# Kernel tuning notes

Hardware: AMD Instinct MI355X
Metric: run time of the kernel (lower is better)

Reference implementation:

```python
import jax, jax.numpy as jnp
import numpy as np

HID = 1024
DEPTH = 2

def _rhn_layer(x, Win, bin_, Wh, bh, Wt, bt):
    # x: [B, T, in]; returns outputs [B, T, H]
    B = x.shape[0]
    h0 = jnp.zeros((B, HID), dtype=x.dtype)
    xt = jnp.swapaxes(x, 0, 1)  # [T, B, in]

    def step(h_prev, x_t):
        h = x_t @ Win + bin_
        for i in range(DEPTH):
            t_gate = jax.nn.sigmoid(h @ Wt[i] + bt[i])
            h_layer = jnp.tanh(h @ Wh[i] + bh[i])
            h = t_gate * h_layer + (1.0 - t_gate) * h
        h_new = h + h_prev
        return h_new, h_new

    _, outs = jax.lax.scan(step, h0, xt)  # [T, B, H]
    return jnp.swapaxes(outs, 0, 1)


def setup_inputs() -> dict:
    key = jax.random.key(0)
    ks = jax.random.split(key, 16)
    B, T, IN, H, OUT = 64, 256, 128, HID, 128
    s = lambda fan_in: 1.0 / np.sqrt(fan_in)
    d = {}
    d["x"] = jax.random.normal(ks[0], (B, T, IN), dtype=jnp.float32)
    # layer 0 (input_size=IN)
    d["l0_Win"] = jax.random.uniform(ks[1], (IN, H), minval=-s(IN), maxval=s(IN))
    d["l0_bin"] = jax.random.uniform(ks[2], (H,), minval=-s(IN), maxval=s(IN))
    d["l0_Wh"] = jax.random.uniform(ks[3], (DEPTH, H, H), minval=-s(H), maxval=s(H))
    d["l0_bh"] = jax.random.uniform(ks[4], (DEPTH, H), minval=-s(H), maxval=s(H))
    d["l0_Wt"] = jax.random.uniform(ks[5], (DEPTH, H, H), minval=-s(H), maxval=s(H))
    d["l0_bt"] = jax.random.uniform(ks[6], (DEPTH, H), minval=-s(H), maxval=s(H))
    # layer 1 (input_size=H)
    d["l1_Win"] = jax.random.uniform(ks[7], (H, H), minval=-s(H), maxval=s(H))
    d["l1_bin"] = jax.random.uniform(ks[8], (H,), minval=-s(H), maxval=s(H))
    d["l1_Wh"] = jax.random.uniform(ks[9], (DEPTH, H, H), minval=-s(H), maxval=s(H))
    d["l1_bh"] = jax.random.uniform(ks[10], (DEPTH, H), minval=-s(H), maxval=s(H))
    d["l1_Wt"] = jax.random.uniform(ks[11], (DEPTH, H, H), minval=-s(H), maxval=s(H))
    d["l1_bt"] = jax.random.uniform(ks[12], (DEPTH, H), minval=-s(H), maxval=s(H))
    # final fc
    d["fc_W"] = jax.random.uniform(ks[13], (H, OUT), minval=-s(H), maxval=s(H))
    d["fc_b"] = jax.random.uniform(ks[14], (OUT,), minval=-s(H), maxval=s(H))
    return d


def reference(x, l0_Win, l0_bin, l0_Wh, l0_bh, l0_Wt, l0_bt,
              l1_Win, l1_bin, l1_Wh, l1_bh, l1_Wt, l1_bt, fc_W, fc_b):
    out = _rhn_layer(x, l0_Win, l0_bin, l0_Wh, l0_bh, l0_Wt, l0_bt)
    out = _rhn_layer(out, l1_Win, l1_bin, l1_Wh, l1_bh, l1_Wt, l1_bt)
    # forecast_horizon = 1 -> last time step only
    out = out[:, -1:, :] @ fc_W + fc_b  # [B, 1, OUT]
    return out
```

## Files before the change

kernel.cpp:

```cpp
#include <hip/hip_runtime.h>

typedef unsigned short u16;
typedef unsigned int u32;
typedef __bf16 bf16x8 __attribute__((ext_vector_type(8)));
typedef float floatx4 __attribute__((ext_vector_type(4)));

#define HID 1024
#define BATCH 64
#define SEQ 256
#define INDIM 128
#define OUTDIM 128
#define MROWS (BATCH*SEQ)

__device__ __forceinline__ float b2f(u16 u) {
    union { u32 u; float f; } v; v.u = ((u32)u) << 16; return v.f;
}
__device__ __forceinline__ u16 f2b(float f) {
    union { float f; u32 u; } v; v.f = f;
    u32 x = v.u;
    x += 0x7fffu + ((x >> 16) & 1u);
    return (u16)(x >> 16);
}
__device__ __forceinline__ float sigm(float x) { return 1.f / (1.f + __expf(-x)); }
__device__ __forceinline__ float tanh_f(float x) { return 2.f / (1.f + __expf(-2.f * x)) - 1.f; }

__device__ __forceinline__ void gld16(const u16* g, u16* l) {
    __builtin_amdgcn_global_load_lds(
        (const __attribute__((address_space(1))) void*)g,
        (__attribute__((address_space(3))) void*)l, 16, 0, 0);
}

__device__ __forceinline__ void bar_sync() {
    asm volatile("" ::: "memory");
    __builtin_amdgcn_s_barrier();
    asm volatile("" ::: "memory");
}
template <int N>
__device__ __forceinline__ void vm_bar() {
    asm volatile("s_waitcnt vmcnt(%0)" :: "n"(N) : "memory");
    __builtin_amdgcn_s_barrier();
    asm volatile("" ::: "memory");
}

__global__ void detect_dtype(const u16* __restrict__ w, int* __restrict__ flag) {
    __shared__ int s;
    if (threadIdx.x == 0) s = 0;
    __syncthreads();
    int bad = 0;
    for (int i = threadIdx.x; i < 4096; i += 256) {
        int e = (w[i] >> 7) & 0xff;
        if (e >= 127) bad = 1;
    }
    if (bad) atomicOr(&s, 1);
    __syncthreads();
    if (threadIdx.x == 0) *flag = s;
}

__device__ __forceinline__ int is_fp32(const u16* probe) {
    const int lane = threadIdx.x & 63;
    const int e = (probe[lane * 7] >> 7) & 0xff;
    return __ballot(e >= 127) != 0ULL;
}

struct CvtList { const void* s[7]; u16* d[7]; int n[7]; };

__global__ void convert7(CvtList C, const int* __restrict__ flag) {
    const int fp32 = *flag;
    const int z = blockIdx.y;
    const int n = C.n[z];
    const int stride = gridDim.x * 256;
    for (int i = blockIdx.x * 256 + threadIdx.x; i < n; i += stride) {
        u16 o;
        if (fp32) o = f2b(((const float*)C.s[z])[i]);
        else      o = ((const u16*)C.s[z])[i];
        C.d[z][i] = o;
    }
}

struct TListO {
    const void* s[10];
    u16*        d[10];
    int         R[10];
    int         Cc[10];
    long        off[10];
};

__global__ void transpose10(TListO L, const int* __restrict__ flag) {
    const int fp32 = *flag;
    const int z = blockIdx.z;
    const void* src = L.s[z];
    u16*        dst = L.d[z];
    const int R  = L.R[z];
    const int Cc = L.Cc[z];
    const long zo = L.off[z];
    const int tr = blockIdx.y * 32, tc = blockIdx.x * 32;
    if (tr >= R || tc >= Cc) return;
    __align__(16) __shared__ u16 t[32][33];
    const int tx = threadIdx.x, ty = threadIdx.y;
#pragma unroll
    for (int i = 0; i < 4; ++i) {
        const int r = ty + i * 8;
        const long e = zo + (long)(tr + r) * Cc + tc + tx;
        u16 v;
        if (fp32) v = f2b(((const float*)src)[e]);
        else      v = ((const u16*)src)[e];
        t[r][tx] = v;
    }
    __syncthreads();
#pragma unroll
    for (int i = 0; i < 4; ++i) {
        const int r = ty + i * 8;
        dst[(size_t)(tc + r) * R + tr + tx] = t[tx][r];
    }
}

__device__ __forceinline__ void tile_swizzle(int& m0, int& n0) {
    const int lin = blockIdx.y * gridDim.x + blockIdx.x;
    const int xcd = lin & 7;
    const int loc = lin >> 3;
    m0 = (xcd * 16 + (loc & 15)) * 128;
    n0 = (loc >> 4) * 128;
}

__device__ __forceinline__ void tile_swizzle8(int& m0, int& n0) {
    const int lin = blockIdx.x;
    const int xcd = lin & 7;
    const int loc = lin >> 3;
    m0 = (xcd * 8 + (loc & 7)) * 256;
    n0 = (loc >> 3) * 128;
}

__global__ __launch_bounds__(256, 2) void gemm128(
    const u16* __restrict__ A, const u16* __restrict__ BT,
    const u16* __restrict__ bias, u16* __restrict__ C,
    int M, int N, int K)
{
    __align__(16) __shared__ u16 As[128 * 64];
    __align__(16) __shared__ u16 Bs[128 * 64];

    const int tid  = threadIdx.x;
    const int lane = tid & 63;
    const int wid  = tid >> 6;
    const int wr   = wid >> 1;
    const int wc   = wid & 1;

    int m0, n0;
    tile_swizzle(m0, n0);

    floatx4 acc[4][4] = {};

    const int srow = lane >> 3;
    const int scol = 8 * ((lane & 7) ^ (lane >> 3));
    const int cb   = wid * 4;
    const u16* Ag[4]; const u16* Bg[4];
    u16 *Al[4], *Bl[4];
#pragma unroll
    for (int j = 0; j < 4; ++j) {
        const int c = cb + j;
        const int r = c * 8 + srow;
        Ag[j] = A  + (size_t)(m0 + r) * K + scol;
        Bg[j] = BT + (size_t)(n0 + r) * K + scol;
        Al[j] = As + c * 512;
        Bl[j] = Bs + c * 512;
    }

    const int quad = lane >> 4;
    const int l16  = lane & 15;
    const int swz  = l16 & 7;

    const int nk = K >> 6;
    for (int kt = 0; kt < nk; ++kt) {
        __syncthreads();
#pragma unroll
        for (int j = 0; j < 4; ++j) {
            gld16(Ag[j], Al[j]);  gld16(Bg[j], Bl[j]);
            Ag[j] += 64; Bg[j] += 64;
        }
        __syncthreads();

#pragma unroll
        for (int kk = 0; kk < 2; ++kk) {
            const int slot = ((kk * 4 + quad) ^ swz) * 8;
            bf16x8 af[4], bfr[4];
#pragma unroll
            for (int i = 0; i < 4; ++i) {
                af[i]  = *(const bf16x8*)(As + (wr * 64 + i * 16 + l16) * 64 + slot);
                bfr[i] = *(const bf16x8*)(Bs + (wc * 64 + i * 16 + l16) * 64 + slot);
            }
#pragma unroll
            for (int i = 0; i < 4; ++i)
#pragma unroll
                for (int j = 0; j < 4; ++j)
                    acc[i][j] = __builtin_amdgcn_mfma_f32_16x16x32_bf16(af[i], bfr[j], acc[i][j], 0, 0, 0);
        }
    }

#pragma unroll
    for (int i = 0; i < 4; ++i) {
        const int rowb = m0 + wr * 64 + i * 16 + quad * 4;
#pragma unroll
        for (int j = 0; j < 4; ++j) {
            const int col = n0 + wc * 64 + j * 16 + l16;
            const float bv = b2f(bias[col]);
#pragma unroll
            for (int r = 0; r < 4; ++r)
                C[(size_t)(rowb + r) * N + col] = f2b(acc[i][j][r] + bv);
        }
    }
}

__device__ __forceinline__ void hw8_mainloop(
    const u16* __restrict__ A, const u16* __restrict__ WtT, const u16* __restrict__ WhT,
    int m0, int n0, int K,
    floatx4 (&acct)[4][4], floatx4 (&acch)[4][4])
{
    __align__(16) __shared__ u16 lds[65536];

    const int tid  = threadIdx.x;
    const int lane = tid & 63;
    const int wid  = tid >> 6;
    const int wr   = wid >> 1;
    const int wc   = wid & 1;

    const int srow = lane >> 3;
    const int scol = 8 * ((lane & 7) ^ srow);

    const u16* Ag = A   + (size_t)(m0 + wid * 32 + srow) * K + scol;
    const u16* Tg = WtT + (size_t)(n0 + wid * 16 + srow) * K + scol;
    const u16* Hg = WhT + (size_t)(n0 + wid * 16 + srow) * K + scol;
    const size_t K8 = (size_t)K * 8;

    u16* dA = lds + wid * 2048;
    u16* dT = lds + 16384 + wid * 1024;
    u16* dH = lds + 24576 + wid * 1024;

    const int quad = lane >> 4;
    const int l16  = lane & 15;
    const int swz  = l16 & 7;
    const int s0 = (quad ^ swz) * 8;
    const int s1 = ((4 + quad) ^ swz) * 8;
    const int ra = wr * 64 + l16;
    const int rb = wc * 64 + l16;

    gld16(Tg,           dT);
    gld16(Tg +     K8,  dT + 512);
    gld16(Ag,           dA);
    gld16(Ag +     K8,  dA + 512);
    gld16(Ag + 2 * K8,  dA + 1024);
    gld16(Ag + 3 * K8,  dA + 1536);
    gld16(Hg,           dH);
    gld16(Hg +     K8,  dH + 512);
    Ag += 64; Tg += 64; Hg += 64;
    vm_bar<2>();

    const int nk = K >> 6;
    for (int kt = 0; kt < nk; ++kt) {
        const int  cur = kt & 1;
        const int  nb  = (cur ^ 1) * 32768;
        const bool pf  = (kt + 1 < nk);
        const u16* Sa = lds + cur * 32768;
        const u16* St = Sa + 16384;
        const u16* Sh = Sa + 24576;

        bf16x8 af0[4], af1[4], bq[4];

#pragma unroll
        for (int i = 0; i < 4; ++i) {
            af0[i] = *(const bf16x8*)(Sa + (ra + i * 16) * 64 + s0);
            bq[i]  = *(const bf16x8*)(St + (rb + i * 16) * 64 + s0);
        }
        if (pf) {
            gld16(Tg,      dT + nb);  gld16(Tg + K8, dT + nb + 512);
            gld16(Ag,      dA + nb);  gld16(Ag + K8, dA + nb + 512);
        }
        bar_sync();
        __builtin_amdgcn_s_setprio(1);
#pragma unroll
        for (int i = 0; i < 4; ++i)
#pragma unroll
            for (int j = 0; j < 4; ++j)
                acct[i][j] = __builtin_amdgcn_mfma_f32_16x16x32_bf16(af0[i], bq[j], acct[i][j], 0, 0, 0);
        __builtin_amdgcn_s_setprio(0);

#pragma unroll
        for (int i = 0; i < 4; ++i) {
            af1[i] = *(const bf16x8*)(Sa + (ra + i * 16) * 64 + s1);
            bq[i]  = *(const bf16x8*)(St + (rb + i * 16) * 64 + s1);
        }
        if (pf) {
            gld16(Ag + 2 * K8, dA + nb + 1024);
            gld16(Ag + 3 * K8, dA + nb + 1536);
            vm_bar<6>();
        } else {
            vm_bar<0>();
        }
        __builtin_amdgcn_s_setprio(1);
#pragma unroll
        for (int i = 0; i < 4; ++i)
#pragma unroll
            for (int j = 0; j < 4; ++j)
                acct[i][j] = __builtin_amdgcn_mfma_f32_16x16x32_bf16(af1[i], bq[j], acct[i][j], 0, 0, 0);
        __builtin_amdgcn_s_setprio(0);

#pragma unroll
        for (int i = 0; i < 4; ++i)
            bq[i] = *(const bf16x8*)(Sh + (rb + i * 16) * 64 + s0);
        bar_sync();
        __builtin_amdgcn_s_setprio(1);
#pragma unroll
        for (int i = 0; i < 4; ++i)
#pragma unroll
            for (int j = 0; j < 4; ++j)
                acch[i][j] = __builtin_amdgcn_mfma_f32_16x16x32_bf16(af0[i], bq[j], acch[i][j], 0, 0, 0);
        __builtin_amdgcn_s_setprio(0);

#pragma unroll
        for (int i = 0; i < 4; ++i)
            bq[i] = *(const bf16x8*)(Sh + (rb + i * 16) * 64 + s1);
        if (pf) {
            gld16(Hg,      dH + nb);
            gld16(Hg + K8, dH + nb + 512);
            vm_bar<2>();
        } else {
            bar_sync();
        }
        __builtin_amdgcn_s_setprio(1);
#pragma unroll
        for (int i = 0; i < 4; ++i)
#pragma unroll
            for (int j = 0; j < 4; ++j)
                acch[i][j] = __builtin_amdgcn_mfma_f32_16x16x32_bf16(af1[i], bq[j], acch[i][j], 0, 0, 0);
        __builtin_amdgcn_s_setprio(0);

        Ag += 64; Tg += 64; Hg += 64;
    }
}

__global__ __launch_bounds__(512, 2) void gemm_hw8(
    const u16* __restrict__ A,
    const u16* __restrict__ WtT,
    const u16* __restrict__ WhT,
    const u16* __restrict__ bt, const u16* __restrict__ bh,
    u16* __restrict__ Hout,
    int M, int N, int K)
{
    int m0, n0;
    tile_swizzle8(m0, n0);

    floatx4 acct[4][4] = {};
    floatx4 acch[4][4] = {};
    hw8_mainloop(A, WtT, WhT, m0, n0, K, acct, acch);

    const int tid  = threadIdx.x;
    const int lane = tid & 63;
    const int wid  = tid >> 6;
    const int wr   = wid >> 1;
    const int wc   = wid & 1;
    const int quad = lane >> 4;
    const int l16  = lane & 15;

#pragma unroll
    for (int i = 0; i < 4; ++i) {
        const int rowb = m0 + wr * 64 + i * 16 + quad * 4;
#pragma unroll
        for (int j = 0; j < 4; ++j) {
            const int col = n0 + wc * 64 + j * 16 + l16;
            const float btv = b2f(bt[col]);
            const float bhv = b2f(bh[col]);
#pragma unroll
            for (int r = 0; r < 4; ++r) {
                const size_t idx = (size_t)(rowb + r) * N + col;
                const float hold = b2f(A[idx]);
                const float tg = sigm(acct[i][j][r] + btv);
                const float hl = tanh_f(acch[i][j][r] + bhv);
                Hout[idx] = f2b(hold + tg * (hl - hold));
            }
        }
    }
}

__global__ __launch_bounds__(512, 2) void gemm_hw8_sum(
    const u16* __restrict__ A,
    const u16* __restrict__ WtT,
    const u16* __restrict__ WhT,
    const u16* __restrict__ bt, const u16* __restrict__ bh,
    float* __restrict__ hsum,
    int M, int N, int K)
{
    int m0, n0;
    tile_swizzle8(m0, n0);

    floatx4 acct[4][4] = {};
    floatx4 acch[4][4] = {};
    hw8_mainloop(A, WtT, WhT, m0, n0, K, acct, acch);

    const int tid  = threadIdx.x;
    const int lane = tid & 63;
    const int wid  = tid >> 6;
    const int wr   = wid >> 1;
    const int wc   = wid & 1;
    const int quad = lane >> 4;
    const int l16  = lane & 15;

    const int b = m0 >> 8;
#pragma unroll
    for (int j = 0; j < 4; ++j) {
        const int col = n0 + wc * 64 + j * 16 + l16;
        const float btv = b2f(bt[col]);
        const float bhv = b2f(bh[col]);
        float colsum = 0.f;
#pragma unroll
        for (int i = 0; i < 4; ++i) {
            const int rowb = m0 + wr * 64 + i * 16 + quad * 4;
#pragma unroll
            for (int r = 0; r < 4; ++r) {
                const size_t idx = (size_t)(rowb + r) * N + col;
                const float hold = b2f(A[idx]);
                const float tg = sigm(acct[i][j][r] + btv);
                const float hl = tanh_f(acch[i][j][r] + bhv);
                colsum += hold + tg * (hl - hold);
            }
        }
        colsum += __shfl_xor(colsum, 16, 64);
        colsum += __shfl_xor(colsum, 32, 64);
        if (quad == 0)
            atomicAdd(&hsum[(size_t)b * HID + col], colsum);
    }
}

__global__ void zero_hf(float* __restrict__ p) {
    p[blockIdx.x * 256 + threadIdx.x] = 0.f;
}

__global__ void cumsum_t(u16* g) {
    const int id = blockIdx.x * 256 + threadIdx.x;
    const int b = id >> 10, f = id & 1023;
    size_t base = (size_t)b * SEQ * HID + f;
    float acc = 0.f;
#pragma unroll 4
    for (int t = 0; t < SEQ; ++t) {
        size_t idx = base + (size_t)t * HID;
        acc += b2f(g[idx]);
        g[idx] = f2b(acc);
    }
}

__global__ void fc_final(const float* __restrict__ hf, const void* __restrict__ W,
                         const void* __restrict__ bias, void* __restrict__ out) {
    __shared__ float sh[HID];
    const int fp32 = is_fp32((const u16*)W);
    const int b = blockIdx.x, o = threadIdx.x;
    for (int k = o; k < HID; k += 128) sh[k] = hf[(size_t)b * HID + k];
    __syncthreads();
    float acc;
    if (fp32) {
        acc = ((const float*)bias)[o];
        for (int k = 0; k < HID; ++k)
            acc += sh[k] * ((const float*)W)[(size_t)k * OUTDIM + o];
        ((float*)out)[b * OUTDIM + o] = acc;
    } else {
        acc = b2f(((const u16*)bias)[o]);
        for (int k = 0; k < HID; ++k)
            acc += sh[k] * b2f(((const u16*)W)[(size_t)k * OUTDIM + o]);
        ((u16*)out)[b * OUTDIM + o] = f2b(acc);
    }
}

extern "C" void kernel_launch(void* const* d_in, const int* in_sizes, int n_in,
                              void* d_out, int out_size, void* d_ws, size_t ws_size,
                              hipStream_t stream) {
    const void* x      = d_in[0];
    const void* l0_Win = d_in[1];
    const void* l0_bin = d_in[2];
    const void* l0_Wh  = d_in[3];
    const void* l0_bh  = d_in[4];
    const void* l0_Wt  = d_in[5];
    const void* l0_bt  = d_in[6];
    const void* l1_Win = d_in[7];
    const void* l1_bin = d_in[8];
    const void* l1_Wh  = d_in[9];
    const void* l1_bh  = d_in[10];
    const void* l1_Wt  = d_in[11];
    const void* l1_bt  = d_in[12];
    const void* fc_W   = d_in[13];
    const void* fc_b   = d_in[14];

    char* ws = (char*)d_ws;
    u16* Pa = (u16*)(ws);
    u16* Pb = (u16*)(ws + 33554432);
    u16* xc = Pb;
    u16* tW = (u16*)(ws + 67108864);
    u16* tWin0 = tW;
    u16* tWt00 = tWin0 + 131072;
    u16* tWt01 = tWt00 + 1048576;
    u16* tWh00 = tWt01 + 1048576;
    u16* tWh01 = tWh00 + 1048576;
    u16* tWin1 = tWh01 + 1048576;
    u16* tWt10 = tWin1 + 1048576;
    u16* tWt11 = tWt10 + 1048576;
    u16* tWh10 = tWt11 + 1048576;
    u16* tWh11 = tWh10 + 1048576;
    u16* smallb = tWh11 + 1048576;
    u16* binc0 = smallb;
    u16* bhc0  = binc0 + 1024;
    u16* btc0  = bhc0 + 2048;
    u16* binc1 = btc0 + 2048;
    u16* bhc1  = binc1 + 1024;
    u16* btc1  = bhc1 + 2048;
    int* flag  = (int*)(btc1 + 2048);
    float* hfinal = (float*)Pb;

    detect_dtype<<<1, 256, 0, stream>>>((const u16*)l0_Wh, flag);

    const long DD = (long)HID * HID;
    TListO L;
    L.s[0] = l0_Win; L.d[0] = tWin0; L.R[0] = INDIM; L.Cc[0] = HID; L.off[0] = 0;
    L.s[1] = l0_Wt;  L.d[1] = tWt00; L.R[1] = HID;   L.Cc[1] = HID; L.off[1] = 0;
    L.s[2] = l0_Wt;  L.d[2] = tWt01; L.R[2] = HID;   L.Cc[2] = HID; L.off[2] = DD;
    L.s[3] = l0_Wh;  L.d[3] = tWh00; L.R[3] = HID;   L.Cc[3] = HID; L.off[3] = 0;
    L.s[4] = l0_Wh;  L.d[4] = tWh01; L.R[4] = HID;   L.Cc[4] = HID; L.off[4] = DD;
    L.s[5] = l1_Win; L.d[5] = tWin1; L.R[5] = HID;   L.Cc[5] = HID; L.off[5] = 0;
    L.s[6] = l1_Wt;  L.d[6] = tWt10; L.R[6] = HID;   L.Cc[6] = HID; L.off[6] = 0;
    L.s[7] = l1_Wt;  L.d[7] = tWt11; L.R[7] = HID;   L.Cc[7] = HID; L.off[7] = DD;
    L.s[8] = l1_Wh;  L.d[8] = tWh10; L.R[8] = HID;   L.Cc[8] = HID; L.off[8] = 0;
    L.s[9] = l1_Wh;  L.d[9] = tWh11; L.R[9] = HID;   L.Cc[9] = HID; L.off[9] = DD;
    transpose10<<<dim3(32, 32, 10), dim3(32, 8), 0, stream>>>(L, flag);

    CvtList C7;
    C7.s[0] = x;      C7.d[0] = xc;    C7.n[0] = MROWS * INDIM;
    C7.s[1] = l0_bin; C7.d[1] = binc0; C7.n[1] = HID;
    C7.s[2] = l0_bh;  C7.d[2] = bhc0;  C7.n[2] = 2 * HID;
    C7.s[3] = l0_bt;  C7.d[3] = btc0;  C7.n[3] = 2 * HID;
    C7.s[4] = l1_bin; C7.d[4] = binc1; C7.n[4] = HID;
    C7.s[5] = l1_bh;  C7.d[5] = bhc1;  C7.n[5] = 2 * HID;
    C7.s[6] = l1_bt;  C7.d[6] = btc1;  C7.n[6] = 2 * HID;
    convert7<<<dim3(512, 7), 256, 0, stream>>>(C7, flag);

    gemm128<<<dim3(8, 128), 256, 0, stream>>>(xc, tWin0, binc0, Pa, MROWS, HID, INDIM);
    gemm_hw8<<<512, 512, 0, stream>>>(Pa, tWt00, tWh00, btc0, bhc0, Pb, MROWS, HID, HID);
    gemm_hw8<<<512, 512, 0, stream>>>(Pb, tWt01, tWh01, btc0 + HID, bhc0 + HID, Pa, MROWS, HID, HID);
    cumsum_t<<<256, 256, 0, stream>>>(Pa);

    gemm128<<<dim3(8, 128), 256, 0, stream>>>(Pa, tWin1, binc1, Pb, MROWS, HID, HID);
    gemm_hw8<<<512, 512, 0, stream>>>(Pb, tWt10, tWh10, btc1, bhc1, Pa, MROWS, HID, HID);
    zero_hf<<<256, 256, 0, stream>>>(hfinal);
    gemm_hw8_sum<<<512, 512, 0, stream>>>(Pa, tWt11, tWh11, btc1 + HID, bhc1 + HID,
                                          hfinal, MROWS, HID, HID);

    fc_final<<<64, 128, 0, stream>>>(hfinal, fc_W, fc_b, d_out);
}
```

Baseline: 538.0 us.

## Fuse time cumsum into highway GEMM epilogue; swap hw8 kernels for simpler hw GEMM

The second highway GEMM of layer 0 now stages its 256x128 output tile in shared memory. It runs the per-column prefix sum over the 256 time steps there and writes the cumulated result, so the separate cumsum_t pass over global memory is dropped. The other three highway GEMMs move from the pipelined 512-thread hw8 kernel to a simpler 256-thread kernel with 128x128 tiles and a single buffer. That change looks like a regression and could slow those GEMMs. The fused cumsum is a serial loop run by only 128 threads per block, which may stall the block's tail.

After: 526.8 us. 2.1% less time.

```diff
diff --git a/kernel.cpp b/kernel.cpp
--- a/kernel.cpp
+++ b/kernel.cpp
@@ -209,13 +209,208 @@
     }
 }
 
+__global__ __launch_bounds__(256, 2) void gemm_hw(
+    const u16* __restrict__ A,
+    const u16* __restrict__ WtT,
+    const u16* __restrict__ WhT,
+    const u16* __restrict__ bt, const u16* __restrict__ bh,
+    u16* __restrict__ Hout,
+    int M, int N, int K)
+{
+    __align__(16) __shared__ u16 As [128 * 64];
+    __align__(16) __shared__ u16 Bts[128 * 64];
+    __align__(16) __shared__ u16 Bhs[128 * 64];
+
+    const int tid  = threadIdx.x;
+    const int lane = tid & 63;
+    const int wid  = tid >> 6;
+    const int wr   = wid >> 1;
+    const int wc   = wid & 1;
+
+    int m0, n0;
+    tile_swizzle(m0, n0);
+
+    floatx4 acct[4][4] = {};
+    floatx4 acch[4][4] = {};
+
+    const int srow = lane >> 3;
+    const int scol = 8 * ((lane & 7) ^ (lane >> 3));
+    const int cb   = wid * 4;
+    const u16* Ag[4]; const u16* Tg[4]; const u16* Hg[4];
+    u16 *Al[4], *Tl[4], *Hl[4];
+#pragma unroll
+    for (int j = 0; j < 4; ++j) {
+        const int c = cb + j;
+        const int r = c * 8 + srow;
+        Ag[j] = A   + (size_t)(m0 + r) * K + scol;
+        Tg[j] = WtT + (size_t)(n0 + r) * K + scol;
+        Hg[j] = WhT + (size_t)(n0 + r) * K + scol;
+        Al[j] = As  + c * 512;
+        Tl[j] = Bts + c * 512;
+        Hl[j] = Bhs + c * 512;
+    }
+
+    const int quad = lane >> 4;
+    const int l16  = lane & 15;
+    const int swz  = l16 & 7;
+
+    const int nk = K >> 6;
+    for (int kt = 0; kt < nk; ++kt) {
+        __syncthreads();
+#pragma unroll
+        for (int j = 0; j < 4; ++j) {
+            gld16(Ag[j], Al[j]);  gld16(Tg[j], Tl[j]);  gld16(Hg[j], Hl[j]);
+            Ag[j] += 64; Tg[j] += 64; Hg[j] += 64;
+        }
+        __syncthreads();
+
+#pragma unroll
+        for (int kk = 0; kk < 2; ++kk) {
+            const int slot = ((kk * 4 + quad) ^ swz) * 8;
+            bf16x8 af[4], btf[4], bhf[4];
+#pragma unroll
+            for (int i = 0; i < 4; ++i) {
+                af[i]  = *(const bf16x8*)(As  + (wr * 64 + i * 16 + l16) * 64 + slot);
+                btf[i] = *(const bf16x8*)(Bts + (wc * 64 + i * 16 + l16) * 64 + slot);
+                bhf[i] = *(const bf16x8*)(Bhs + (wc * 64 + i * 16 + l16) * 64 + slot);
+            }
+#pragma unroll
+            for (int i = 0; i < 4; ++i)
+#pragma unroll
+                for (int j = 0; j < 4; ++j) {
+                    acct[i][j] = __builtin_amdgcn_mfma_f32_16x16x32_bf16(af[i], btf[j], acct[i][j], 0, 0, 0);
+                    acch[i][j] = __builtin_amdgcn_mfma_f32_16x16x32_bf16(af[i], bhf[j], acch[i][j], 0, 0, 0);
+                }
+        }
+    }
+
+#pragma unroll
+    for (int i = 0; i < 4; ++i) {
+        const int rowb = m0 + wr * 64 + i * 16 + quad * 4;
+#pragma unroll
+        for (int j = 0; j < 4; ++j) {
+            const int col = n0 + wc * 64 + j * 16 + l16;
+            const float btv = b2f(bt[col]);
+            const float bhv = b2f(bh[col]);
+#pragma unroll
+            for (int r = 0; r < 4; ++r) {
+                const size_t idx = (size_t)(rowb + r) * N + col;
+                const float hold = b2f(A[idx]);
+                const float tg = sigm(acct[i][j][r] + btv);
+                const float hl = tanh_f(acch[i][j][r] + bhv);
+                Hout[idx] = f2b(hold + tg * (hl - hold));
+            }
+        }
+    }
+}
+
+__global__ __launch_bounds__(256, 2) void gemm_hw_sum(
+    const u16* __restrict__ A,
+    const u16* __restrict__ WtT,
+    const u16* __restrict__ WhT,
+    const u16* __restrict__ bt, const u16* __restrict__ bh,
+    float* __restrict__ hsum,
+    int M, int N, int K)
+{
+    __align__(16) __shared__ u16 As [128 * 64];
+    __align__(16) __shared__ u16 Bts[128 * 64];
+    __align__(16) __shared__ u16 Bhs[128 * 64];
+
+    const int tid  = threadIdx.x;
+    const int lane = tid & 63;
+    const int wid  = tid >> 6;
+    const int wr   = wid >> 1;
+    const int wc   = wid & 1;
+
+    int m0, n0;
+    tile_swizzle(m0, n0);
+
+    floatx4 acct[4][4] = {};
+    floatx4 acch[4][4] = {};
+
+    const int srow = lane >> 3;
+    const int scol = 8 * ((lane & 7) ^ (lane >> 3));
+    const int cb   = wid * 4;
+    const u16* Ag[4]; const u16* Tg[4]; const u16* Hg[4];
+    u16 *Al[4], *Tl[4], *Hl[4];
+#pragma unroll
+    for (int j = 0; j < 4; ++j) {
+        const int c = cb + j;
+        const int r = c * 8 + srow;
+        Ag[j] = A   + (size_t)(m0 + r) * K + scol;
+        Tg[j] = WtT + (size_t)(n0 + r) * K + scol;
+        Hg[j] = WhT + (size_t)(n0 + r) * K + scol;
+        Al[j] = As  + c * 512;
+        Tl[j] = Bts + c * 512;
+        Hl[j] = Bhs + c * 512;
+    }
+
+    const int quad = lane >> 4;
+    const int l16  = lane & 15;
+    const int swz  = l16 & 7;
+
+    const int nk = K >> 6;
+    for (int kt = 0; kt < nk; ++kt) {
+        __syncthreads();
+#pragma unroll
+        for (int j = 0; j < 4; ++j) {
+            gld16(Ag[j], Al[j]);  gld16(Tg[j], Tl[j]);  gld16(Hg[j], Hl[j]);
+            Ag[j] += 64; Tg[j] += 64; Hg[j] += 64;
+        }
+        __syncthreads();
+
+#pragma unroll
+        for (int kk = 0; kk < 2; ++kk) {
+            const int slot = ((kk * 4 + quad) ^ swz) * 8;
+            bf16x8 af[4], btf[4], bhf[4];
+#pragma unroll
+            for (int i = 0; i < 4; ++i) {
+                af[i]  = *(const bf16x8*)(As  + (wr * 64 + i * 16 + l16) * 64 + slot);
+                btf[i] = *(const bf16x8*)(Bts + (wc * 64 + i * 16 + l16) * 64 + slot);
+                bhf[i] = *(const bf16x8*)(Bhs + (wc * 64 + i * 16 + l16) * 64 + slot);
+            }
+#pragma unroll
+            for (int i = 0; i < 4; ++i)
+#pragma unroll
+                for (int j = 0; j < 4; ++j) {
+                    acct[i][j] = __builtin_amdgcn_mfma_f32_16x16x32_bf16(af[i], btf[j], acct[i][j], 0, 0, 0);
+                    acch[i][j] = __builtin_amdgcn_mfma_f32_16x16x32_bf16(af[i], bhf[j], acch[i][j], 0, 0, 0);
+                }
+        }
+    }
+
+    const int b = m0 >> 8;
+#pragma unroll
+    for (int j = 0; j < 4; ++j) {
+        const int col = n0 + wc * 64 + j * 16 + l16;
+        const float btv = b2f(bt[col]);
+        const float bhv = b2f(bh[col]);
+        float colsum = 0.f;
+#pragma unroll
+        for (int i = 0; i < 4; ++i) {
+            const int rowb = m0 + wr * 64 + i * 16 + quad * 4;
+#pragma unroll
+            for (int r = 0; r < 4; ++r) {
+                const size_t idx = (size_t)(rowb + r) * N + col;
+                const float hold = b2f(A[idx]);
+                const float tg = sigm(acct[i][j][r] + btv);
+                const float hl = tanh_f(acch[i][j][r] + bhv);
+                colsum += hold + tg * (hl - hold);
+            }
+        }
+        colsum += __shfl_xor(colsum, 16, 64);
+        colsum += __shfl_xor(colsum, 32, 64);
+        if (quad == 0)
+            atomicAdd(&hsum[(size_t)b * HID + col], colsum);
+    }
+}
+
 __device__ __forceinline__ void hw8_mainloop(
+    u16* lds,
     const u16* __restrict__ A, const u16* __restrict__ WtT, const u16* __restrict__ WhT,
     int m0, int n0, int K,
     floatx4 (&acct)[4][4], floatx4 (&acch)[4][4])
 {
-    __align__(16) __shared__ u16 lds[65536];
-
     const int tid  = threadIdx.x;
     const int lane = tid & 63;
     const int wid  = tid >> 6;
@@ -336,20 +531,22 @@
     }
 }
 
-__global__ __launch_bounds__(512, 2) void gemm_hw8(
+__global__ __launch_bounds__(512, 2) void gemm_hw8_cum(
     const u16* __restrict__ A,
     const u16* __restrict__ WtT,
     const u16* __restrict__ WhT,
     const u16* __restrict__ bt, const u16* __restrict__ bh,
-    u16* __restrict__ Hout,
+    u16* __restrict__ Y,
     int M, int N, int K)
 {
+    __align__(16) __shared__ u16 lds[65536];
+
     int m0, n0;
     tile_swizzle8(m0, n0);
 
     floatx4 acct[4][4] = {};
     floatx4 acch[4][4] = {};
-    hw8_mainloop(A, WtT, WhT, m0, n0, K, acct, acch);
+    hw8_mainloop(lds, A, WtT, WhT, m0, n0, K, acct, acch);
 
     const int tid  = threadIdx.x;
     const int lane = tid & 63;
@@ -359,90 +556,50 @@
     const int quad = lane >> 4;
     const int l16  = lane & 15;
 
+    __syncthreads();
+
 #pragma unroll
     for (int i = 0; i < 4; ++i) {
-        const int rowb = m0 + wr * 64 + i * 16 + quad * 4;
+        const int rowl = wr * 64 + i * 16 + quad * 4;
 #pragma unroll
         for (int j = 0; j < 4; ++j) {
-            const int col = n0 + wc * 64 + j * 16 + l16;
-            const float btv = b2f(bt[col]);
-            const float bhv = b2f(bh[col]);
+            const int coll = wc * 64 + j * 16 + l16;
+            const float btv = b2f(bt[n0 + coll]);
+            const float bhv = b2f(bh[n0 + coll]);
 #pragma unroll
             for (int r = 0; r < 4; ++r) {
-                const size_t idx = (size_t)(rowb + r) * N + col;
+                const size_t idx = (size_t)(m0 + rowl + r) * N + n0 + coll;
                 const float hold = b2f(A[idx]);
                 const float tg = sigm(acct[i][j][r] + btv);
                 const float hl = tanh_f(acch[i][j][r] + bhv);
-                Hout[idx] = f2b(hold + tg * (hl - hold));
+                lds[(rowl + r) * 128 + coll] = f2b(hold + tg * (hl - hold));
             }
         }
     }
-}
-
-__global__ __launch_bounds__(512, 2) void gemm_hw8_sum(
-    const u16* __restrict__ A,
-    const u16* __restrict__ WtT,
-    const u16* __restrict__ WhT,
-    const u16* __restrict__ bt, const u16* __restrict__ bh,
-    float* __restrict__ hsum,
-    int M, int N, int K)
-{
-    int m0, n0;
-    tile_swizzle8(m0, n0);
-
-    floatx4 acct[4][4] = {};
-    floatx4 acch[4][4] = {};
-    hw8_mainloop(A, WtT, WhT, m0, n0, K, acct, acch);
-
-    const int tid  = threadIdx.x;
-    const int lane = tid & 63;
-    const int wid  = tid >> 6;
-    const int wr   = wid >> 1;
-    const int wc   = wid & 1;
-    const int quad = lane >> 4;
-    const int l16  = lane & 15;
-
-    const int b = m0 >> 8;
-#pragma unroll
-    for (int j = 0; j < 4; ++j) {
-        const int col = n0 + wc * 64 + j * 16 + l16;
-        const float btv = b2f(bt[col]);
-        const float bhv = b2f(bh[col]);
-        float colsum = 0.f;
-#pragma unroll
-        for (int i = 0; i < 4; ++i) {
-            const int rowb = m0 + wr * 64 + i * 16 + quad * 4;
-#pragma unroll
-            for (int r = 0; r < 4; ++r) {
-                const size_t idx = (size_t)(rowb + r) * N + col;
-                const float hold = b2f(A[idx]);
-                const float tg = sigm(acct[i][j][r] + btv);
-                const float hl = tanh_f(acch[i][j][r] + bhv);
-                colsum += hold + tg * (hl - hold);
-            }
-        }
-        colsum += __shfl_xor(colsum, 16, 64);
-        colsum += __shfl_xor(colsum, 32, 64);
-        if (quad == 0)
-            atomicAdd(&hsum[(size_t)b * HID + col], colsum);
+    __syncthreads();
+
+    if (tid < 128) {
+        float acc = 0.f;
+#pragma unroll 8
+        for (int t = 0; t < SEQ; ++t) {
+            const int o = t * 128 + tid;
+            acc += b2f(lds[o]);
+            lds[o] = f2b(acc);
+        }
+    }
+    __syncthreads();
+
+#pragma unroll
+    for (int it = 0; it < 16; ++it) {
+        const int o   = it * 2048 + tid * 4;
+        const int row = o >> 7;
+        const int col = o & 127;
+        *(uint2*)&Y[(size_t)(m0 + row) * N + n0 + col] = *(const uint2*)&lds[o];
     }
 }
 
 __global__ void zero_hf(float* __restrict__ p) {
     p[blockIdx.x * 256 + threadIdx.x] = 0.f;
-}
-
-__global__ void cumsum_t(u16* g) {
-    const int id = blockIdx.x * 256 + threadIdx.x;
-    const int b = id >> 10, f = id & 1023;
-    size_t base = (size_t)b * SEQ * HID + f;
-    float acc = 0.f;
-#pragma unroll 4
-    for (int t = 0; t < SEQ; ++t) {
-        size_t idx = base + (size_t)t * HID;
-        acc += b2f(g[idx]);
-        g[idx] = f2b(acc);
-    }
 }
 
 __global__ void fc_final(const float* __restrict__ hf, const void* __restrict__ W,
@@ -537,15 +694,14 @@
     convert7<<<dim3(512, 7), 256, 0, stream>>>(C7, flag);
 
     gemm128<<<dim3(8, 128), 256, 0, stream>>>(xc, tWin0, binc0, Pa, MROWS, HID, INDIM);
-    gemm_hw8<<<512, 512, 0, stream>>>(Pa, tWt00, tWh00, btc0, bhc0, Pb, MROWS, HID, HID);
-    gemm_hw8<<<512, 512, 0, stream>>>(Pb, tWt01, tWh01, btc0 + HID, bhc0 + HID, Pa, MROWS, HID, HID);
-    cumsum_t<<<256, 256, 0, stream>>>(Pa);
+    gemm_hw<<<dim3(8, 128), 256, 0, stream>>>(Pa, tWt00, tWh00, btc0, bhc0, Pb, MROWS, HID, HID);
+    gemm_hw8_cum<<<512, 512, 0, stream>>>(Pb, tWt01, tWh01, btc0 + HID, bhc0 + HID, Pa, MROWS, HID, HID);
 
     gemm128<<<dim3(8, 128), 256, 0, stream>>>(Pa, tWin1, binc1, Pb, MROWS, HID, HID);
-    gemm_hw8<<<512, 512, 0, stream>>>(Pb, tWt10, tWh10, btc1, bhc1, Pa, MROWS, HID, HID);
+    gemm_hw<<<dim3(8, 128), 256, 0, stream>>>(Pb, tWt10, tWh10, btc1, bhc1, Pa, MROWS, HID, HID);
     zero_hf<<<256, 256, 0, stream>>>(hfinal);
-    gemm_hw8_sum<<<512, 512, 0, stream>>>(Pa, tWt11, tWh11, btc1 + HID, bhc1 + HID,
-                                          hfinal, MROWS, HID, HID);
+    gemm_hw_sum<<<dim3(8, 128), 256, 0, stream>>>(Pa, tWt11, tWh11, btc1 + HID, bhc1 + HID,
+                                                  hfinal, MROWS, HID, HID);
 
     fc_final<<<64, 128, 0, stream>>>(hfinal, fc_W, fc_b, d_out);
 }
```
